# Optimization experiments

Measured on AMD Instinct MI355X. Metric: run time of the kernel, lower is better.

Reference implementation:

```python
import jax, jax.numpy as jnp
import numpy as np

B, T, C, H = 32, 576, 1024, 16
D = C // H  # head_dim = 64

def setup_inputs() -> dict:
    key = jax.random.key(0)
    ks = jax.random.split(key, 5)
    s = 1.0 / np.sqrt(C)
    return {
        "emb_img": jax.random.normal(ks[0], (B, T, C), dtype=jnp.float32),
        "w_qkv": jax.random.normal(ks[1], (C, 3 * C), dtype=jnp.float32) * s,
        "b_qkv": jnp.zeros((3 * C,), dtype=jnp.float32),
        "w_proj": jax.random.normal(ks[2], (C, C), dtype=jnp.float32) * s,
        "b_proj": jnp.zeros((C,), dtype=jnp.float32),
    }

def reference(emb_img, w_qkv, b_qkv, w_proj, b_proj):
    # fused QKV projection
    qkv = emb_img @ w_qkv + b_qkv                       # [B,T,3C]
    q, k, v = jnp.split(qkv, 3, axis=-1)                # each [B,T,C]
    def heads(x):
        return x.reshape(B, T, H, D).transpose(0, 2, 1, 3)  # [B,H,T,D]
    q, k, v = heads(q), heads(k), heads(v)
    # note: original scales by 1/head_dim (not 1/sqrt(head_dim))
    scores = jnp.einsum("bhqd,bhkd->bhqk", q, k) * (1.0 / D)
    causal = jnp.tril(jnp.ones((T, T), dtype=bool))
    scores = jnp.where(causal[None, None], scores, -jnp.inf)
    att = jax.nn.softmax(scores, axis=-1)               # [B,H,T,T]
    y = jnp.einsum("bhqk,bhkd->bhqd", att, v)           # [B,H,T,D]
    y = y.transpose(0, 2, 1, 3).reshape(B, T, C)
    return y @ w_proj + b_proj
```

## Files before the change

### kernel.cpp

```cpp
#include <hip/hip_runtime.h>
#include <stdint.h>

namespace {

constexpr int kB = 32, kT = 576, kC = 1024, kH = 16, kD = 64;
constexpr int kM = kB * kT;
constexpr int kNqkv = 3 * kC;
constexpr float kQScale = 1.4426950408889634f / 64.0f;

typedef uint16_t u16;
typedef __attribute__((ext_vector_type(4))) float f32x4;
typedef __attribute__((ext_vector_type(8))) short short8;
typedef __attribute__((ext_vector_type(8))) __bf16 bf16x8;
typedef __attribute__((ext_vector_type(4))) uint16_t u16x4;

#define VMCNT(n) asm volatile("s_waitcnt vmcnt(" #n ")" ::: "memory")

__device__ __forceinline__ float fexp2(float x) {
  return __builtin_amdgcn_exp2f(x);
}

__device__ __forceinline__ f32x4 mfma_bf16(short8 a, short8 b, f32x4 c) {
  return __builtin_amdgcn_mfma_f32_16x16x32_bf16(
      __builtin_bit_cast(bf16x8, a), __builtin_bit_cast(bf16x8, b), c, 0, 0, 0);
}

__device__ __forceinline__ u16 to_bf16(float x) {
  uint32_t u = __float_as_uint(x);
  u += 0x7fffu + ((u >> 16) & 1u);
  return (u16)(u >> 16);
}

__device__ __forceinline__ void gload_lds16(const void* g, void* l) {
  __builtin_amdgcn_global_load_lds(
      (const __attribute__((address_space(1))) uint32_t*)(uintptr_t)g,
      (__attribute__((address_space(3))) uint32_t*)(uintptr_t)l,
      16, 0, 0);
}

__device__ __forceinline__ void bar() {
  asm volatile("" ::: "memory");
  __builtin_amdgcn_s_barrier();
  asm volatile("" ::: "memory");
}

__global__ __launch_bounds__(256) void cvt_bf16_kernel(
    const float* __restrict__ in, u16* __restrict__ out, int n4) {
  const int i = blockIdx.x * 256 + threadIdx.x;
  if (i >= n4) return;
  const f32x4 v = ((const f32x4*)in)[i];
  u16x4 o;
#pragma unroll
  for (int j = 0; j < 4; ++j) o[j] = to_bf16(v[j]);
  ((u16x4*)out)[i] = o;
}

__global__ void tconv_kernel(const float* __restrict__ in, u16* __restrict__ out,
                             int K, int N) {
  __shared__ u16 tile[32][33];
  const int nb = blockIdx.x * 32;
  const int kb = blockIdx.y * 32;
  const int tx = threadIdx.x;
  const int ty = threadIdx.y;
#pragma unroll
  for (int i = 0; i < 32; i += 8)
    tile[ty + i][tx] = to_bf16(in[(size_t)(kb + ty + i) * N + nb + tx]);
  __syncthreads();
#pragma unroll
  for (int i = 0; i < 32; i += 8)
    out[(size_t)(nb + ty + i) * K + kb + tx] = tile[tx][ty + i];
}

__global__ __launch_bounds__(512, 2) void gemm_qkv(
    const u16* __restrict__ A, const u16* __restrict__ Bt,
    const float* __restrict__ bias,
    u16* __restrict__ outQ, u16* __restrict__ outK, u16* __restrict__ outVT) {
  constexpr int Kc = 1024;
  constexpr int NT = Kc / 64;
  __shared__ char lds[3][49152];

  const int tid = threadIdx.x;
  const int wave = tid >> 6;
  const int lane = tid & 63;
  const int lo = lane & 15;
  const int hi = lane >> 4;
  const int wr = wave >> 1;
  const int wc = wave & 1;

  const int lin = blockIdx.x + blockIdx.y * 24;
  const int l2 = (lin & 7) * 216 + (lin >> 3);
  const int n0 = (l2 % 24) * 128;
  const int m0 = (l2 / 24) * 256;

  const u16* srcA[4];
  const u16* srcB[2];
#pragma unroll
  for (int c = 0; c < 4; ++c) {
    const int b = c * 8192 + wave * 1024 + lane * 16;
    const int row = b >> 7;
    const int colb = (b & 127) ^ ((row & 7) << 4);
    srcA[c] = A + (size_t)(m0 + row) * Kc + (colb >> 1);
  }
#pragma unroll
  for (int c = 0; c < 2; ++c) {
    const int b = c * 8192 + wave * 1024 + lane * 16;
    const int row = b >> 7;
    const int colb = (b & 127) ^ ((row & 7) << 4);
    srcB[c] = Bt + (size_t)(n0 + row) * Kc + (colb >> 1);
  }

  auto stage = [&](int slot, int t) {
    const int k0 = t * 64;
    char* base = &lds[slot][0];
#pragma unroll
    for (int c = 0; c < 4; ++c)
      gload_lds16(srcA[c] + k0, base + c * 8192 + wave * 1024);
#pragma unroll
    for (int c = 0; c < 2; ++c)
      gload_lds16(srcB[c] + k0, base + 32768 + c * 8192 + wave * 1024);
  };

  f32x4 acc[4][4] = {};

  auto compute = [&](int slot) {
    const char* base = &lds[slot][0];
    __builtin_amdgcn_s_setprio(1);
#pragma unroll
    for (int ks = 0; ks < 2; ++ks) {
      const int cb = (ks * 64 + hi * 16) ^ ((lo & 7) << 4);
      short8 af[4], bfv[4];
#pragma unroll
      for (int i = 0; i < 4; ++i)
        af[i] = *(const short8*)(base + (wr * 64 + i * 16 + lo) * 128 + cb);
#pragma unroll
      for (int j = 0; j < 4; ++j)
        bfv[j] = *(const short8*)(base + 32768 + (wc * 64 + j * 16 + lo) * 128 + cb);
#pragma unroll
      for (int i = 0; i < 4; ++i)
#pragma unroll
        for (int j = 0; j < 4; ++j)
          acc[i][j] = mfma_bf16(af[i], bfv[j], acc[i][j]);
    }
    __builtin_amdgcn_s_setprio(0);
  };

  stage(0, 0);
  stage(1, 1);
  for (int t = 0; t < NT - 2; ++t) {
    stage((t + 2) % 3, t + 2);
    VMCNT(12);
    bar();
    compute(t % 3);
    bar();
  }
  VMCNT(6);
  bar();
  compute((NT - 2) % 3);
  bar();
  VMCNT(0);
  bar();
  compute((NT - 1) % 3);

  if (n0 >= 2048) {
    bar();
    u16* wlds = (u16*)&lds[0][0] + wave * (64 * 66);
    uint32_t* wlds32 = (uint32_t*)wlds;
#pragma unroll
    for (int j = 0; j < 4; ++j) {
      const int n = n0 + wc * 64 + j * 16 + lo;
      const float bv = bias[n];
#pragma unroll
      for (int i = 0; i < 4; ++i)
#pragma unroll
        for (int rp = 0; rp < 2; ++rp) {
          const u16 w0 = to_bf16(acc[i][j][rp * 2] + bv);
          const u16 w1 = to_bf16(acc[i][j][rp * 2 + 1] + bv);
          wlds32[(j * 16 + lo) * 33 + i * 8 + hi * 2 + rp] =
              (uint32_t)w0 | ((uint32_t)w1 << 16);
        }
    }
#pragma unroll
    for (int p = 0; p < 16; ++p) {
      const int d_local = p * 4 + hi;
      const int n = n0 + wc * 64 + d_local;
      const int c = n & 1023;
      const int hh = c >> 6;
      const int d = c & 63;
      const int m = m0 + wr * 64 + lo * 4;
      const int bb = m / kT;
      const int t = m - bb * kT;
      const u16x4 v = *(const u16x4*)&wlds[d_local * 66 + lo * 4];
      *(u16x4*)&outVT[((size_t)(bb * kH + hh) * kD + d) * kT + t] = v;
    }
  } else {
#pragma unroll
    for (int j = 0; j < 4; ++j) {
      const int n = n0 + wc * 64 + j * 16 + lo;
      const float bv = bias[n];
      const int which = n >> 10;
      const int c = n & 1023;
      const int hh = c >> 6;
      const int d = c & 63;
#pragma unroll
      for (int i = 0; i < 4; ++i) {
        const int mrow = m0 + wr * 64 + i * 16 + hi * 4;
#pragma unroll
        for (int r = 0; r < 4; ++r) {
          const int m = mrow + r;
          const int bb = m / kT;
          const int t = m - bb * kT;
          const float v = acc[i][j][r] + bv;
          if (which == 0)
            outQ[((size_t)(bb * kH + hh) * kT + t) * kD + d] = to_bf16(v * kQScale);
          else
            outK[((size_t)(bb * kH + hh) * kT + t) * kD + d] = to_bf16(v);
        }
      }
    }
  }
}

__global__ __launch_bounds__(256, 3) void gemm_proj(
    const u16* __restrict__ A, const u16* __restrict__ Bt,
    const float* __restrict__ bias, float* __restrict__ outF) {
  constexpr int Kc = 1024;
  constexpr int NT = Kc / 32;
  __shared__ char lds[3][16384];

  const int tid = threadIdx.x;
  const int wave = tid >> 6;
  const int lane = tid & 63;
  const int lo = lane & 15;
  const int hi = lane >> 4;
  const int wr = wave >> 1;
  const int wc = wave & 1;

  const int lin = blockIdx.x + blockIdx.y * 8;
  const int l2 = (lin & 7) * 144 + (lin >> 3);
  const int n0 = (l2 & 7) * 128;
  const int m0 = (l2 >> 3) * 128;

  const u16* srcA[2];
  const u16* srcB[2];
#pragma unroll
  for (int c = 0; c < 2; ++c) {
    const int off = c * 4096 + tid * 16;
    const int p = off >> 7;
    const int col = (off & 127) ^ ((p & 7) << 4);
    const int r_ = (col < 64) ? p : p + 64;
    const int k_ = (col & 63) >> 1;
    srcA[c] = A + (size_t)(m0 + r_) * Kc + k_;
    srcB[c] = Bt + (size_t)(n0 + r_) * Kc + k_;
  }

  auto stage = [&](int slot, int t) {
    char* base = &lds[slot][0];
#pragma unroll
    for (int c = 0; c < 2; ++c) {
      gload_lds16(srcA[c] + t * 32, base + c * 4096 + wave * 1024);
      gload_lds16(srcB[c] + t * 32, base + 8192 + c * 4096 + wave * 1024);
    }
  };

  f32x4 acc[4][4] = {};

  auto compute = [&](int slot) {
    const char* base = &lds[slot][0];
    const char* baseB = base + 8192;
    const int swz = (lo & 7) << 4;
    short8 af[4], bf[4];
#pragma unroll
    for (int i = 0; i < 4; ++i)
      af[i] = *(const short8*)(base + (i * 16 + lo) * 128 + ((wr * 64 + hi * 16) ^ swz));
#pragma unroll
    for (int j = 0; j < 4; ++j)
      bf[j] = *(const short8*)(baseB + (j * 16 + lo) * 128 + ((wc * 64 + hi * 16) ^ swz));
    __builtin_amdgcn_s_setprio(1);
#pragma unroll
    for (int i = 0; i < 4; ++i)
#pragma unroll
      for (int j = 0; j < 4; ++j)
        acc[i][j] = mfma_bf16(af[i], bf[j], acc[i][j]);
    __builtin_amdgcn_s_setprio(0);
  };

  stage(0, 0);
  stage(1, 1);
  for (int t = 0; t < NT - 2; ++t) {
    stage((t + 2) % 3, t + 2);
    VMCNT(8);
    bar();
    compute(t % 3);
    bar();
  }
  VMCNT(4);
  bar();
  compute((NT - 2) % 3);
  bar();
  VMCNT(0);
  bar();
  compute((NT - 1) % 3);

#pragma unroll
  for (int j = 0; j < 4; ++j) {
    const int n = n0 + wc * 64 + j * 16 + lo;
    const float bv = bias[n];
#pragma unroll
    for (int i = 0; i < 4; ++i) {
      const int mrow = m0 + wr * 64 + i * 16 + hi * 4;
#pragma unroll
      for (int r = 0; r < 4; ++r)
        outF[(size_t)(mrow + r) * kC + n] = acc[i][j][r] + bv;
    }
  }
}

__global__ __launch_bounds__(256) void attn_kernel(
    const u16* __restrict__ Q, const u16* __restrict__ K,
    const u16* __restrict__ VT, u16* __restrict__ Y) {
  __shared__ u16 P[4][32][72];

  const int idx = blockIdx.x;
  const int qi = 4 - (idx >> 9);
  const int bh = idx & 511;
  const int wave = threadIdx.x >> 6;
  const int lane = threadIdx.x & 63;
  const int lo = lane & 15;
  const int hi = lane >> 4;
  const int q0 = qi * 128 + wave * 32;
  if (q0 >= kT) return;

  const u16* Qb = Q + (size_t)bh * kT * kD;
  const u16* Kb = K + (size_t)bh * kT * kD;
  const u16* Vb = VT + (size_t)bh * kD * kT;

  short8 qf[2][2];
#pragma unroll
  for (int h = 0; h < 2; ++h) {
    const u16* qp = Qb + (q0 + h * 16 + lo) * kD + hi * 8;
    qf[h][0] = *(const short8*)qp;
    qf[h][1] = *(const short8*)(qp + 32);
  }

  f32x4 acc[2][4] = {};
  float mrun[2] = {-3e38f, -3e38f};
  float lsum[2] = {0.f, 0.f};

  short8 kf[4][2];
#pragma unroll
  for (int kc = 0; kc < 4; ++kc) {
    const u16* kp = Kb + (kc * 16 + lo) * kD + hi * 8;
    kf[kc][0] = *(const short8*)kp;
    kf[kc][1] = *(const short8*)(kp + 32);
  }

  const int kv_end = q0 + 32;
  for (int kv = 0; kv < kv_end; kv += 64) {
    f32x4 s[2][4];
#pragma unroll
    for (int kc = 0; kc < 4; ++kc)
#pragma unroll
      for (int h = 0; h < 2; ++h) {
        f32x4 z = {0.f, 0.f, 0.f, 0.f};
        z = mfma_bf16(kf[kc][0], qf[h][0], z);
        z = mfma_bf16(kf[kc][1], qf[h][1], z);
        s[h][kc] = z;
      }
    short8 vf[4][2];
#pragma unroll
    for (int nt = 0; nt < 4; ++nt) {
      const u16* vp = Vb + (nt * 16 + lo) * kT + kv + hi * 8;
      vf[nt][0] = *(const short8*)vp;
      vf[nt][1] = *(const short8*)(vp + 32);
    }
    if (kv + 64 < kv_end) {
#pragma unroll
      for (int kc = 0; kc < 4; ++kc) {
        const u16* kp = Kb + (kv + 64 + kc * 16 + lo) * kD + hi * 8;
        kf[kc][0] = *(const short8*)kp;
        kf[kc][1] = *(const short8*)(kp + 32);
      }
    }
    if (kv + 63 > q0) {
#pragma unroll
      for (int h = 0; h < 2; ++h) {
        const int q = q0 + h * 16 + lo;
#pragma unroll
        for (int kc = 0; kc < 4; ++kc)
#pragma unroll
          for (int r = 0; r < 4; ++r)
            if (kv + kc * 16 + hi * 4 + r > q) s[h][kc][r] = -3e38f;
      }
    }
#pragma unroll
    for (int h = 0; h < 2; ++h) {
      float m01 = fmaxf(fmaxf(s[h][0][0], s[h][0][1]), fmaxf(s[h][0][2], s[h][0][3]));
      float m23 = fmaxf(fmaxf(s[h][1][0], s[h][1][1]), fmaxf(s[h][1][2], s[h][1][3]));
      float m45 = fmaxf(fmaxf(s[h][2][0], s[h][2][1]), fmaxf(s[h][2][2], s[h][2][3]));
      float m67 = fmaxf(fmaxf(s[h][3][0], s[h][3][1]), fmaxf(s[h][3][2], s[h][3][3]));
      float pm = fmaxf(fmaxf(m01, m23), fmaxf(m45, m67));
      pm = fmaxf(pm, __shfl_xor(pm, 16));
      pm = fmaxf(pm, __shfl_xor(pm, 32));
      const float mnew = fmaxf(mrun[h], pm);
      const float corr = fexp2(mrun[h] - mnew);
      mrun[h] = mnew;
      float psum = 0.f;
#pragma unroll
      for (int kc = 0; kc < 4; ++kc) {
        u16x4 pk;
#pragma unroll
        for (int r = 0; r < 4; ++r) {
          const float pv = fexp2(s[h][kc][r] - mnew);
          psum += pv;
          pk[r] = to_bf16(pv);
        }
        *(u16x4*)&P[wave][h * 16 + lo][kc * 16 + hi * 4] = pk;
      }
      lsum[h] = lsum[h] * corr + psum;
#pragma unroll
      for (int nt = 0; nt < 4; ++nt)
#pragma unroll
        for (int r = 0; r < 4; ++r) acc[h][nt][r] *= corr;
    }
    short8 pf[2][2];
#pragma unroll
    for (int h = 0; h < 2; ++h) {
      pf[h][0] = *(const short8*)&P[wave][h * 16 + lo][hi * 8];
      pf[h][1] = *(const short8*)&P[wave][h * 16 + lo][32 + hi * 8];
    }
#pragma unroll
    for (int nt = 0; nt < 4; ++nt)
#pragma unroll
      for (int h = 0; h < 2; ++h) {
        acc[h][nt] = mfma_bf16(pf[h][0], vf[nt][0], acc[h][nt]);
        acc[h][nt] = mfma_bf16(pf[h][1], vf[nt][1], acc[h][nt]);
      }
  }

#pragma unroll
  for (int h = 0; h < 2; ++h) {
    lsum[h] += __shfl_xor(lsum[h], 16);
    lsum[h] += __shfl_xor(lsum[h], 32);
  }
  const int b = bh >> 4, hh = bh & 15;
#pragma unroll
  for (int h = 0; h < 2; ++h)
#pragma unroll
    for (int r = 0; r < 4; ++r) {
      const float linv = 1.0f / __shfl(lsum[h], hi * 4 + r);
      const int t = q0 + h * 16 + hi * 4 + r;
      const size_t base = ((size_t)(b * kT + t) * kH + hh) * kD;
#pragma unroll
      for (int nt = 0; nt < 4; ++nt)
        Y[base + nt * 16 + lo] = to_bf16(acc[h][nt][r] * linv);
    }
}

}

extern "C" void kernel_launch(void* const* d_in, const int* in_sizes, int n_in,
                              void* d_out, int out_size, void* d_ws, size_t ws_size,
                              hipStream_t stream) {
  (void)in_sizes; (void)n_in; (void)out_size; (void)ws_size;
  const float* emb   = (const float*)d_in[0];
  const float* wqkv  = (const float*)d_in[1];
  const float* bqkv  = (const float*)d_in[2];
  const float* wproj = (const float*)d_in[3];
  const float* bproj = (const float*)d_in[4];
  float* out = (float*)d_out;

  char* p = (char*)d_ws;
  u16* embb   = (u16*)p; p += (size_t)kM * kC * 2;
  u16* wqkvt  = (u16*)p; p += (size_t)kNqkv * kC * 2;
  u16* wprojt = (u16*)p; p += (size_t)kC * kC * 2;
  u16* Qh     = (u16*)p; p += (size_t)kM * kC * 2;
  u16* Kh     = (u16*)p; p += (size_t)kM * kC * 2;
  u16* VTh    = (u16*)p; p += (size_t)kM * kC * 2;
  u16* Yh     = (u16*)p; p += (size_t)kM * kC * 2;

  const int n4 = kM * kC / 4;
  cvt_bf16_kernel<<<dim3((n4 + 255) / 256), 256, 0, stream>>>(emb, embb, n4);
  tconv_kernel<<<dim3(kNqkv / 32, kC / 32), dim3(32, 8), 0, stream>>>(wqkv, wqkvt, kC, kNqkv);
  tconv_kernel<<<dim3(kC / 32, kC / 32), dim3(32, 8), 0, stream>>>(wproj, wprojt, kC, kC);
  gemm_qkv<<<dim3(kNqkv / 128, kM / 256), 512, 0, stream>>>(
      embb, wqkvt, bqkv, Qh, Kh, VTh);
  attn_kernel<<<dim3(5 * kB * kH), 256, 0, stream>>>(Qh, Kh, VTh, Yh);
  gemm_proj<<<dim3(kC / 128, kM / 128), 256, 0, stream>>>(
      Yh, wprojt, bproj, out);
}
```

Before: 317.4 us.

## Shrink QKV GEMM K-tile to 32 with double buffering for higher occupancy

Cuts the QKV GEMM's K-step from 64 to 32 and replaces the triple-buffered 48KB-per-stage LDS pipeline with a double-buffered 24KB-per-stage layout. It also raises the launch-bounds occupancy hint from 2 to 4 blocks per CU. The new layout packs the two 32-wide K halves of the tile side by side in a 128-byte swizzled row, and the V-transpose epilogue is split into two passes so it fits in the smaller LDS. The aim is more resident blocks to hide latency, at the cost of twice as many barriers per K, a shallower prefetch depth, and tighter register pressure under the stricter launch bound.

After: 317.7 us. About the same (+0.1%).

```diff
diff --git a/kernel.cpp b/kernel.cpp
--- a/kernel.cpp
+++ b/kernel.cpp
@@ -71,13 +71,13 @@
     out[(size_t)(nb + ty + i) * K + kb + tx] = tile[tx][ty + i];
 }
 
-__global__ __launch_bounds__(512, 2) void gemm_qkv(
+__global__ __launch_bounds__(512, 4) void gemm_qkv(
     const u16* __restrict__ A, const u16* __restrict__ Bt,
     const float* __restrict__ bias,
     u16* __restrict__ outQ, u16* __restrict__ outK, u16* __restrict__ outVT) {
   constexpr int Kc = 1024;
-  constexpr int NT = Kc / 64;
-  __shared__ char lds[3][49152];
+  constexpr int NT = Kc / 32;
+  __shared__ char lds[2][24576];
 
   const int tid = threadIdx.x;
   const int wave = tid >> 6;
@@ -92,105 +92,110 @@
   const int n0 = (l2 % 24) * 128;
   const int m0 = (l2 / 24) * 256;
 
-  const u16* srcA[4];
-  const u16* srcB[2];
-#pragma unroll
-  for (int c = 0; c < 4; ++c) {
-    const int b = c * 8192 + wave * 1024 + lane * 16;
-    const int row = b >> 7;
-    const int colb = (b & 127) ^ ((row & 7) << 4);
-    srcA[c] = A + (size_t)(m0 + row) * Kc + (colb >> 1);
-  }
+  const u16* srcA[2];
 #pragma unroll
   for (int c = 0; c < 2; ++c) {
-    const int b = c * 8192 + wave * 1024 + lane * 16;
-    const int row = b >> 7;
-    const int colb = (b & 127) ^ ((row & 7) << 4);
-    srcB[c] = Bt + (size_t)(n0 + row) * Kc + (colb >> 1);
+    const int off = c * 8192 + tid * 16;
+    const int p = off >> 7;
+    const int col = (off & 127) ^ ((p & 7) << 4);
+    const int Ar = (col < 64) ? p : p + 128;
+    const int k_ = (col & 63) >> 1;
+    srcA[c] = A + (size_t)(m0 + Ar) * Kc + k_;
+  }
+  const u16* srcB1;
+  {
+    const int off = tid * 16;
+    const int p = off >> 7;
+    const int col = (off & 127) ^ ((p & 7) << 4);
+    const int Br = (col < 64) ? p : p + 64;
+    const int k_ = (col & 63) >> 1;
+    srcB1 = Bt + (size_t)(n0 + Br) * Kc + k_;
   }
 
   auto stage = [&](int slot, int t) {
-    const int k0 = t * 64;
     char* base = &lds[slot][0];
-#pragma unroll
-    for (int c = 0; c < 4; ++c)
-      gload_lds16(srcA[c] + k0, base + c * 8192 + wave * 1024);
-#pragma unroll
-    for (int c = 0; c < 2; ++c)
-      gload_lds16(srcB[c] + k0, base + 32768 + c * 8192 + wave * 1024);
+    gload_lds16(srcA[0] + t * 32, base + tid * 16);
+    gload_lds16(srcA[1] + t * 32, base + 8192 + tid * 16);
+    gload_lds16(srcB1 + t * 32, base + 16384 + tid * 16);
   };
 
   f32x4 acc[4][4] = {};
 
   auto compute = [&](int slot) {
     const char* base = &lds[slot][0];
+    const char* baseB = base + 16384;
+    const int swz = (lo & 7) << 4;
+    short8 af[4], bf[4];
+#pragma unroll
+    for (int i = 0; i < 4; ++i) {
+      const int row = wr * 64 + i * 16 + lo;
+      const int prow = row & 127;
+      const int half = row >> 7;
+      af[i] = *(const short8*)(base + prow * 128 + ((half * 64 + hi * 16) ^ swz));
+    }
+#pragma unroll
+    for (int j = 0; j < 4; ++j) {
+      const int row = wc * 64 + j * 16 + lo;
+      const int prow = row & 63;
+      const int half = row >> 6;
+      bf[j] = *(const short8*)(baseB + prow * 128 + ((half * 64 + hi * 16) ^ swz));
+    }
     __builtin_amdgcn_s_setprio(1);
 #pragma unroll
-    for (int ks = 0; ks < 2; ++ks) {
-      const int cb = (ks * 64 + hi * 16) ^ ((lo & 7) << 4);
-      short8 af[4], bfv[4];
-#pragma unroll
-      for (int i = 0; i < 4; ++i)
-        af[i] = *(const short8*)(base + (wr * 64 + i * 16 + lo) * 128 + cb);
+    for (int i = 0; i < 4; ++i)
 #pragma unroll
       for (int j = 0; j < 4; ++j)
-        bfv[j] = *(const short8*)(base + 32768 + (wc * 64 + j * 16 + lo) * 128 + cb);
-#pragma unroll
-      for (int i = 0; i < 4; ++i)
-#pragma unroll
-        for (int j = 0; j < 4; ++j)
-          acc[i][j] = mfma_bf16(af[i], bfv[j], acc[i][j]);
-    }
+        acc[i][j] = mfma_bf16(af[i], bf[j], acc[i][j]);
     __builtin_amdgcn_s_setprio(0);
   };
 
   stage(0, 0);
-  stage(1, 1);
-  for (int t = 0; t < NT - 2; ++t) {
-    stage((t + 2) % 3, t + 2);
-    VMCNT(12);
+  for (int t = 0; t < NT; ++t) {
+    if (t + 1 < NT) {
+      stage((t + 1) & 1, t + 1);
+      VMCNT(3);
+    } else {
+      VMCNT(0);
+    }
     bar();
-    compute(t % 3);
+    compute(t & 1);
     bar();
   }
-  VMCNT(6);
-  bar();
-  compute((NT - 2) % 3);
-  bar();
-  VMCNT(0);
-  bar();
-  compute((NT - 1) % 3);
 
   if (n0 >= 2048) {
-    bar();
-    u16* wlds = (u16*)&lds[0][0] + wave * (64 * 66);
+    u16* wlds = (u16*)&lds[0][0] + wave * (32 * 66);
     uint32_t* wlds32 = (uint32_t*)wlds;
 #pragma unroll
-    for (int j = 0; j < 4; ++j) {
-      const int n = n0 + wc * 64 + j * 16 + lo;
-      const float bv = bias[n];
-#pragma unroll
-      for (int i = 0; i < 4; ++i)
-#pragma unroll
-        for (int rp = 0; rp < 2; ++rp) {
-          const u16 w0 = to_bf16(acc[i][j][rp * 2] + bv);
-          const u16 w1 = to_bf16(acc[i][j][rp * 2 + 1] + bv);
-          wlds32[(j * 16 + lo) * 33 + i * 8 + hi * 2 + rp] =
-              (uint32_t)w0 | ((uint32_t)w1 << 16);
-        }
-    }
-#pragma unroll
-    for (int p = 0; p < 16; ++p) {
-      const int d_local = p * 4 + hi;
-      const int n = n0 + wc * 64 + d_local;
-      const int c = n & 1023;
-      const int hh = c >> 6;
-      const int d = c & 63;
-      const int m = m0 + wr * 64 + lo * 4;
-      const int bb = m / kT;
-      const int t = m - bb * kT;
-      const u16x4 v = *(const u16x4*)&wlds[d_local * 66 + lo * 4];
-      *(u16x4*)&outVT[((size_t)(bb * kH + hh) * kD + d) * kT + t] = v;
+    for (int jp = 0; jp < 2; ++jp) {
+#pragma unroll
+      for (int jj = 0; jj < 2; ++jj) {
+        const int j = jp * 2 + jj;
+        const int n = n0 + wc * 64 + j * 16 + lo;
+        const float bv = bias[n];
+        const int dl = jj * 16 + lo;
+#pragma unroll
+        for (int i = 0; i < 4; ++i)
+#pragma unroll
+          for (int rp = 0; rp < 2; ++rp) {
+            const u16 w0 = to_bf16(acc[i][j][rp * 2] + bv);
+            const u16 w1 = to_bf16(acc[i][j][rp * 2 + 1] + bv);
+            wlds32[dl * 33 + i * 8 + hi * 2 + rp] =
+                (uint32_t)w0 | ((uint32_t)w1 << 16);
+          }
+      }
+#pragma unroll
+      for (int p = 0; p < 8; ++p) {
+        const int dl32 = p * 4 + hi;
+        const int n = n0 + wc * 64 + jp * 32 + dl32;
+        const int c = n & 1023;
+        const int hh = c >> 6;
+        const int d = c & 63;
+        const int m = m0 + wr * 64 + lo * 4;
+        const int bb = m / kT;
+        const int t = m - bb * kT;
+        const u16x4 v = *(const u16x4*)&wlds[dl32 * 66 + lo * 4];
+        *(u16x4*)&outVT[((size_t)(bb * kH + hh) * kD + d) * kT + t] = v;
+      }
     }
   } else {
 #pragma unroll
```
